# Performance work log

Hardware: AMD Instinct MI355X
Metric: run time of the kernel (lower is better)

The kernel has to match this reference:

```python
import jax, jax.numpy as jnp
import numpy as np

ALPHA = 0.2  # LeakyReLU negative slope


def setup_inputs() -> dict:
    key = jax.random.key(0)
    ks = jax.random.split(key, 8)
    B, S, T, V, F = 8, 25, 64, 256, 256
    N = S * T
    h = jax.random.normal(ks[0], (B, S, T, V), dtype=jnp.float32)
    adj = jax.random.randint(ks[1], (N, N), 0, 2, dtype=jnp.int32)
    # xavier-ish scaling for stability
    W = jax.random.normal(ks[2], (F, V), dtype=jnp.float32) * (1.414 / np.sqrt(V))
    bW = jax.random.normal(ks[3], (F,), dtype=jnp.float32) * 0.01
    ai = jax.random.normal(ks[4], (1, F), dtype=jnp.float32) * (1.414 / np.sqrt(F))
    bi = jax.random.normal(ks[5], (1,), dtype=jnp.float32) * 0.01
    aj = jax.random.normal(ks[6], (1, F), dtype=jnp.float32) * (1.414 / np.sqrt(F))
    bj = jax.random.normal(ks[7], (1,), dtype=jnp.float32) * 0.01
    return {"h": h, "adj": adj, "W": W, "bW": bW, "ai": ai, "bi": bi, "aj": aj, "bj": bj}


def reference(h, adj, W, bW, ai, bi, aj, bj):
    B, S, T, V = h.shape
    N = S * T
    x = h.reshape(B, N, V)                    # [B, N, V]
    Wh = jnp.einsum('bnv,fv->bnf', x, W) + bW  # [B, N, F]
    Wh1 = jnp.einsum('bnf,of->bno', Wh, ai) + bi  # [B, N, 1]
    Wh2 = jnp.einsum('bnf,of->bno', Wh, aj) + bj  # [B, N, 1]
    e = Wh1 + jnp.swapaxes(Wh2, 1, 2)          # [B, N, N] additive scores
    e = jnp.where(e > 0, e, ALPHA * e)         # LeakyReLU
    att = jnp.where(adj[None, :, :] > 0, e, jnp.float32(-1e9))
    att = jax.nn.softmax(att, axis=2)          # masked softmax over neighbors
    h_hat = jnp.einsum('bij,bjf->bif', att, Wh)  # [B, N, F]
    return jax.nn.elu(h_hat)                   # concat=True path
```

## Files before the change

### kernel.cpp

```cpp
#include <hip/hip_runtime.h>
#include <hip/hip_bf16.h>

typedef __attribute__((ext_vector_type(8))) short bf16x8;
typedef __attribute__((ext_vector_type(4))) float f32x4;

#define LRELU_ALPHA 0.2f

static __device__ __forceinline__ unsigned short f2bf(float x) {
    unsigned u = __float_as_uint(x);
    u += 0x7fffu + ((u >> 16) & 1u);
    return (unsigned short)(u >> 16);
}
static __device__ __forceinline__ unsigned f2ord(float x) {
    unsigned b = __float_as_uint(x);
    return (b & 0x80000000u) ? ~b : (b | 0x80000000u);
}
static __device__ __forceinline__ float ord2f(unsigned m) {
    unsigned b = (m & 0x80000000u) ? (m ^ 0x80000000u) : ~m;
    return __uint_as_float(b);
}

__global__ __launch_bounds__(256) void k_convert(
    const float* __restrict__ x, const float* __restrict__ W,
    unsigned short* __restrict__ xb, unsigned short* __restrict__ Wb)
{
    const int bid = blockIdx.x;
    const float* src;
    unsigned short* dst;
    size_t base;
    if (bid < 1600) { src = x; dst = xb; base = (size_t)bid * 2048; }
    else            { src = W; dst = Wb; base = (size_t)(bid - 1600) * 2048; }
    const size_t idx = base + (size_t)threadIdx.x * 8;
    float4 v0 = *(const float4*)&src[idx];
    float4 v1 = *(const float4*)&src[idx + 4];
    ushort4 o0 = { f2bf(v0.x), f2bf(v0.y), f2bf(v0.z), f2bf(v0.w) };
    ushort4 o1 = { f2bf(v1.x), f2bf(v1.y), f2bf(v1.z), f2bf(v1.w) };
    *(ushort4*)&dst[idx]     = o0;
    *(ushort4*)&dst[idx + 4] = o1;
}

__global__ __launch_bounds__(256) void k_gemm_fused(
    const unsigned short* __restrict__ xb, const unsigned short* __restrict__ Wb,
    const float* __restrict__ bW, const float* __restrict__ ai,
    const float* __restrict__ bi, const float* __restrict__ aj,
    const float* __restrict__ bj,
    unsigned short* __restrict__ WhT, float* __restrict__ Wh1,
    float* __restrict__ Wh2, unsigned* __restrict__ M2g)
{
    __shared__ float part1[2][32], part2[2][32];
    const int t = threadIdx.x;
    const int w = t >> 6, l = t & 63;
    const int wr = w >> 1, wc = w & 1;
    const int R0 = blockIdx.x * 32;
    const int arow = R0 + wr*16 + (l & 15);
    const int kg8 = (l >> 4) * 8;

    f32x4 acc[8];
#pragma unroll
    for (int nf = 0; nf < 8; ++nf) acc[nf] = (f32x4){0.f,0.f,0.f,0.f};

#pragma unroll 2
    for (int k0 = 0; k0 < 256; k0 += 32) {
        bf16x8 af = *(const bf16x8*)&xb[(size_t)arow*256 + k0 + kg8];
#pragma unroll
        for (int nf = 0; nf < 8; ++nf) {
            bf16x8 bfv = *(const bf16x8*)&Wb[(size_t)(wc*128 + nf*16 + (l&15))*256 + k0 + kg8];
            acc[nf] = __builtin_amdgcn_mfma_f32_16x16x32_bf16(af, bfv, acc[nf], 0, 0, 0);
        }
    }

    const int b   = R0 / 1600;
    const int n0b = R0 - b*1600;
    const int rowg = wr*16 + (l>>4)*4;
    float p1[4] = {0,0,0,0}, p2[4] = {0,0,0,0};
#pragma unroll
    for (int nf = 0; nf < 8; ++nf) {
        const int f = wc*128 + nf*16 + (l & 15);
        const float bwv = bW[f], aiv = ai[f], ajv = aj[f];
        float vv[4];
#pragma unroll
        for (int e = 0; e < 4; ++e) {
            float v = acc[nf][e] + bwv;
            vv[e] = v;
            p1[e] = __builtin_fmaf(v, aiv, p1[e]);
            p2[e] = __builtin_fmaf(v, ajv, p2[e]);
        }
        ushort4 o4 = { f2bf(vv[0]), f2bf(vv[1]), f2bf(vv[2]), f2bf(vv[3]) };
        *(ushort4*)&WhT[((size_t)(b*256 + f))*1600 + n0b + rowg] = o4;
    }
#pragma unroll
    for (int m = 1; m < 16; m <<= 1)
#pragma unroll
        for (int e = 0; e < 4; ++e) {
            p1[e] += __shfl_xor(p1[e], m, 64);
            p2[e] += __shfl_xor(p2[e], m, 64);
        }
    if ((l & 15) == 0)
#pragma unroll
        for (int e = 0; e < 4; ++e) {
            part1[wc][rowg + e] = p1[e];
            part2[wc][rowg + e] = p2[e];
        }
    __syncthreads();
    if (t < 32) {
        float v1 = part1[0][t] + part1[1][t] + bi[0];
        float v2 = part2[0][t] + part2[1][t] + bj[0];
        Wh1[R0 + t] = v1;
        Wh2[R0 + t] = v2;
        unsigned o = f2ord(v2);
#pragma unroll
        for (int m = 1; m < 32; m <<= 1) {
            unsigned o2 = __shfl_xor(o, m, 64);
            o = (o2 > o) ? o2 : o;
        }
        if (t == 0) atomicMax(&M2g[b], o);
    }
}

__global__ __launch_bounds__(512) void k_attn(
    const unsigned short* __restrict__ WhT,
    const float* __restrict__ Wh1, const unsigned* __restrict__ M2g,
    const float* __restrict__ Wh2, const int* __restrict__ adj,
    float* __restrict__ out)
{
    __shared__ alignas(16) unsigned short pls[2][32*64];
    __shared__ float l_s[32];

    const int t = threadIdx.x;
    const int w = t >> 6, l = t & 63;
    const int b = blockIdx.x & 7;
    const int i0 = (blockIdx.x >> 3) * 32;

    const float m2v = ord2f(M2g[b]);
    float wh1r[4], mr[4];
#pragma unroll
    for (int r = 0; r < 4; ++r) {
        int gi = i0 + w*4 + r;
        wh1r[r] = Wh1[b*1600 + gi];
        float s = wh1r[r] + m2v;
        mr[r] = s > 0.f ? s : LRELU_ALPHA * s;
    }
    float lsum[4] = {0.f,0.f,0.f,0.f};
    f32x4 acc[2][2];
#pragma unroll
    for (int mi = 0; mi < 2; ++mi)
#pragma unroll
        for (int nf = 0; nf < 2; ++nf) acc[mi][nf] = (f32x4){0.f,0.f,0.f,0.f};

    const unsigned short* whtb = WhT + (size_t)b*256*1600;
    const unsigned short* bp0 = whtb + (size_t)(w*32 +  0 + (l&15))*1600 + (l>>4)*8;
    const unsigned short* bp1 = whtb + (size_t)(w*32 + 16 + (l&15))*1600 + (l>>4)*8;

    int ac[4]; float wcur; bf16x8 bc[2][2];
#pragma unroll
    for (int r = 0; r < 4; ++r) ac[r] = adj[(size_t)(i0 + w*4 + r)*1600 + l];
    wcur = Wh2[b*1600 + l];
    bc[0][0] = *(const bf16x8*)(bp0);      bc[0][1] = *(const bf16x8*)(bp0 + 32);
    bc[1][0] = *(const bf16x8*)(bp1);      bc[1][1] = *(const bf16x8*)(bp1 + 32);

    for (int jt = 0; jt < 25; ++jt) {
        const int cb = jt & 1;
        int an[4]; float wn; bf16x8 bn[2][2];
        if (jt < 24) {
            const int j1 = (jt + 1) * 64;
            bn[0][0] = *(const bf16x8*)(bp0 + j1);      bn[0][1] = *(const bf16x8*)(bp0 + j1 + 32);
            bn[1][0] = *(const bf16x8*)(bp1 + j1);      bn[1][1] = *(const bf16x8*)(bp1 + j1 + 32);
#pragma unroll
            for (int r = 0; r < 4; ++r)
                an[r] = adj[(size_t)(i0 + w*4 + r)*1600 + j1 + l];
            wn = Wh2[b*1600 + j1 + l];
        }
        __builtin_amdgcn_sched_barrier(0);
#pragma unroll
        for (int r = 0; r < 4; ++r) {
            const int row = w*4 + r;
            float s = wh1r[r] + wcur;
            s = s > 0.f ? s : LRELU_ALPHA * s;
            float p = (ac[r] > 0) ? __expf(s - mr[r]) : 0.f;
            lsum[r] += p;
            int off = (row*128 + l*2) ^ ((row & 7) << 4);
            *(unsigned short*)((char*)pls[cb] + off) = f2bf(p);
        }
        asm volatile("s_waitcnt lgkmcnt(0)" ::: "memory");
        __builtin_amdgcn_sched_barrier(0);
        __builtin_amdgcn_s_barrier();
#pragma unroll
        for (int kb = 0; kb < 2; ++kb) {
            bf16x8 af[2];
#pragma unroll
            for (int mi = 0; mi < 2; ++mi) {
                int ar = mi*16 + (l & 15);
                int aoff = (ar*128 + kb*64 + (l>>4)*16) ^ ((ar & 7) << 4);
                af[mi] = *(const bf16x8*)((const char*)pls[cb] + aoff);
            }
#pragma unroll
            for (int mi = 0; mi < 2; ++mi)
#pragma unroll
                for (int nf = 0; nf < 2; ++nf)
                    acc[mi][nf] = __builtin_amdgcn_mfma_f32_16x16x32_bf16(
                        af[mi], bc[nf][kb], acc[mi][nf], 0, 0, 0);
        }
        if (jt < 24) {
#pragma unroll
            for (int r = 0; r < 4; ++r) ac[r] = an[r];
            wcur = wn;
#pragma unroll
            for (int nf = 0; nf < 2; ++nf)
#pragma unroll
                for (int kb = 0; kb < 2; ++kb) bc[nf][kb] = bn[nf][kb];
        }
    }
#pragma unroll
    for (int s2 = 1; s2 < 64; s2 <<= 1)
#pragma unroll
        for (int r = 0; r < 4; ++r)
            lsum[r] += __shfl_xor(lsum[r], s2, 64);
    if (l == 0)
#pragma unroll
        for (int r = 0; r < 4; ++r) l_s[w*4 + r] = lsum[r];
    __syncthreads();
#pragma unroll
    for (int mi = 0; mi < 2; ++mi)
#pragma unroll
        for (int e = 0; e < 4; ++e) {
            const int row = mi*16 + (l>>4)*4 + e;
            const float rl = 1.f / l_s[row];
#pragma unroll
            for (int nf = 0; nf < 2; ++nf) {
                float v = acc[mi][nf][e] * rl;
                v = v > 0.f ? v : expm1f(v);
                out[(size_t)(b*1600 + i0 + row)*256 + w*32 + nf*16 + (l & 15)] = v;
            }
        }
}

extern "C" void kernel_launch(void* const* d_in, const int* in_sizes, int n_in,
                              void* d_out, int out_size, void* d_ws, size_t ws_size,
                              hipStream_t stream)
{
    const float* h  = (const float*)d_in[0];
    const int* adj  = (const int*)d_in[1];
    const float* W  = (const float*)d_in[2];
    const float* bW = (const float*)d_in[3];
    const float* ai = (const float*)d_in[4];
    const float* bi = (const float*)d_in[5];
    const float* aj = (const float*)d_in[6];
    const float* bj = (const float*)d_in[7];
    float* out = (float*)d_out;

    char* ws = (char*)d_ws;
    unsigned short* xb  = (unsigned short*)ws;
    unsigned short* Wb  = (unsigned short*)(ws + 6553600);
    unsigned short* WhT = (unsigned short*)(ws + 6684672);
    float* Wh1 = (float*)(ws + 13238272);
    float* Wh2 = (float*)(ws + 13289472);
    unsigned* M2g = (unsigned*)(ws + 13340672);

    hipMemsetAsync(M2g, 0, 32, stream);
    k_convert<<<1632, 256, 0, stream>>>(h, W, xb, Wb);
    k_gemm_fused<<<400, 256, 0, stream>>>(xb, Wb, bW, ai, bi, aj, bj,
                                          WhT, Wh1, Wh2, M2g);
    k_attn<<<400, 512, 0, stream>>>(WhT, Wh1, M2g, Wh2, adj, out);
}
```

Measured before the change: 162.2 us.

## Split attention over key halves with combine kernel; halve GEMM row tile

The attention kernel now splits the 25 key tiles into two halves handled by separate blocks, doubling the grid to 800 blocks. Each block writes unnormalised partial outputs and row sums to workspace, and a new final kernel adds them, normalises and applies ELU. The projection GEMM uses 16-row tiles across 800 blocks, and the attention loop is restructured into a two-stage unrolled load/compute pipeline. This targets low occupancy on a GPU with many CUs, at the cost of roughly 26 MB of extra partial-result traffic and one more launch.

```diff
diff --git a/kernel.cpp b/kernel.cpp
--- a/kernel.cpp
+++ b/kernel.cpp
@@ -47,35 +47,34 @@
     unsigned short* __restrict__ WhT, float* __restrict__ Wh1,
     float* __restrict__ Wh2, unsigned* __restrict__ M2g)
 {
-    __shared__ float part1[2][32], part2[2][32];
+    __shared__ float part1[4][16], part2[4][16];
     const int t = threadIdx.x;
     const int w = t >> 6, l = t & 63;
-    const int wr = w >> 1, wc = w & 1;
-    const int R0 = blockIdx.x * 32;
-    const int arow = R0 + wr*16 + (l & 15);
+    const int R0 = blockIdx.x * 16;
+    const int arow = R0 + (l & 15);
     const int kg8 = (l >> 4) * 8;
 
-    f32x4 acc[8];
-#pragma unroll
-    for (int nf = 0; nf < 8; ++nf) acc[nf] = (f32x4){0.f,0.f,0.f,0.f};
-
-#pragma unroll 2
+    f32x4 acc[4];
+#pragma unroll
+    for (int nf = 0; nf < 4; ++nf) acc[nf] = (f32x4){0.f,0.f,0.f,0.f};
+
+#pragma unroll
     for (int k0 = 0; k0 < 256; k0 += 32) {
         bf16x8 af = *(const bf16x8*)&xb[(size_t)arow*256 + k0 + kg8];
 #pragma unroll
-        for (int nf = 0; nf < 8; ++nf) {
-            bf16x8 bfv = *(const bf16x8*)&Wb[(size_t)(wc*128 + nf*16 + (l&15))*256 + k0 + kg8];
+        for (int nf = 0; nf < 4; ++nf) {
+            bf16x8 bfv = *(const bf16x8*)&Wb[(size_t)(w*64 + nf*16 + (l&15))*256 + k0 + kg8];
             acc[nf] = __builtin_amdgcn_mfma_f32_16x16x32_bf16(af, bfv, acc[nf], 0, 0, 0);
         }
     }
 
     const int b   = R0 / 1600;
     const int n0b = R0 - b*1600;
-    const int rowg = wr*16 + (l>>4)*4;
+    const int rowg = (l >> 4) * 4;
     float p1[4] = {0,0,0,0}, p2[4] = {0,0,0,0};
 #pragma unroll
-    for (int nf = 0; nf < 8; ++nf) {
-        const int f = wc*128 + nf*16 + (l & 15);
+    for (int nf = 0; nf < 4; ++nf) {
+        const int f = w*64 + nf*16 + (l & 15);
         const float bwv = bW[f], aiv = ai[f], ajv = aj[f];
         float vv[4];
 #pragma unroll
@@ -98,22 +97,74 @@
     if ((l & 15) == 0)
 #pragma unroll
         for (int e = 0; e < 4; ++e) {
-            part1[wc][rowg + e] = p1[e];
-            part2[wc][rowg + e] = p2[e];
+            part1[w][rowg + e] = p1[e];
+            part2[w][rowg + e] = p2[e];
         }
     __syncthreads();
-    if (t < 32) {
-        float v1 = part1[0][t] + part1[1][t] + bi[0];
-        float v2 = part2[0][t] + part2[1][t] + bj[0];
+    if (t < 16) {
+        float v1 = part1[0][t]+part1[1][t]+part1[2][t]+part1[3][t] + bi[0];
+        float v2 = part2[0][t]+part2[1][t]+part2[2][t]+part2[3][t] + bj[0];
         Wh1[R0 + t] = v1;
         Wh2[R0 + t] = v2;
         unsigned o = f2ord(v2);
 #pragma unroll
-        for (int m = 1; m < 32; m <<= 1) {
+        for (int m = 1; m < 16; m <<= 1) {
             unsigned o2 = __shfl_xor(o, m, 64);
             o = (o2 > o) ? o2 : o;
         }
         if (t == 0) atomicMax(&M2g[b], o);
+    }
+}
+
+struct Tile { bf16x8 B[2][2]; int a[4]; float wv; };
+
+static __device__ __forceinline__ void load_tile(
+    Tile& S, int jt, const unsigned short* bp0, const unsigned short* bp1,
+    const int* ap, const float* wh2p, int w)
+{
+    const int j0 = jt * 64;
+    S.B[0][0] = *(const bf16x8*)(bp0 + j0);
+    S.B[0][1] = *(const bf16x8*)(bp0 + j0 + 32);
+    S.B[1][0] = *(const bf16x8*)(bp1 + j0);
+    S.B[1][1] = *(const bf16x8*)(bp1 + j0 + 32);
+#pragma unroll
+    for (int r = 0; r < 4; ++r)
+        S.a[r] = ap[(size_t)(w*4 + r)*1600 + j0];
+    S.wv = wh2p[j0];
+}
+
+static __device__ __forceinline__ void comp_tile(
+    const Tile& S, unsigned short* pb, const float* wh1r, const float* mr,
+    float* lsum, f32x4 (&acc)[2][2], int w, int l)
+{
+#pragma unroll
+    for (int r = 0; r < 4; ++r) {
+        const int row = w*4 + r;
+        float s = wh1r[r] + S.wv;
+        s = s > 0.f ? s : LRELU_ALPHA * s;
+        float p = (S.a[r] > 0) ? __expf(s - mr[r]) : 0.f;
+        lsum[r] += p;
+        int off = (row*128 + l*2) ^ ((row & 7) << 4);
+        *(unsigned short*)((char*)pb + off) = f2bf(p);
+    }
+    asm volatile("s_waitcnt lgkmcnt(0)" ::: "memory");
+    __builtin_amdgcn_sched_barrier(0);
+    __builtin_amdgcn_s_barrier();
+#pragma unroll
+    for (int kb = 0; kb < 2; ++kb) {
+        bf16x8 af[2];
+#pragma unroll
+        for (int mi = 0; mi < 2; ++mi) {
+            int ar = mi*16 + (l & 15);
+            int aoff = (ar*128 + kb*64 + (l>>4)*16) ^ ((ar & 7) << 4);
+            af[mi] = *(const bf16x8*)((const char*)pb + aoff);
+        }
+#pragma unroll
+        for (int mi = 0; mi < 2; ++mi)
+#pragma unroll
+            for (int nf = 0; nf < 2; ++nf)
+                acc[mi][nf] = __builtin_amdgcn_mfma_f32_16x16x32_bf16(
+                    af[mi], S.B[nf][kb], acc[mi][nf], 0, 0, 0);
     }
 }
 
@@ -121,15 +172,20 @@
     const unsigned short* __restrict__ WhT,
     const float* __restrict__ Wh1, const unsigned* __restrict__ M2g,
     const float* __restrict__ Wh2, const int* __restrict__ adj,
-    float* __restrict__ out)
+    float* __restrict__ Oacc, float* __restrict__ Lacc)
 {
     __shared__ alignas(16) unsigned short pls[2][32*64];
-    __shared__ float l_s[32];
 
     const int t = threadIdx.x;
     const int w = t >> 6, l = t & 63;
-    const int b = blockIdx.x & 7;
-    const int i0 = (blockIdx.x >> 3) * 32;
+    const int b  = blockIdx.x & 7;
+    const int r3 = blockIdx.x >> 3;
+    const int js = (r3 >= 50) ? 1 : 0;
+    const int gx = r3 - js*50;
+    const int i0 = gx * 32;
+    const int ggid = b*50 + gx;
+    const int t0   = js ? 13 : 0;
+    const int tend = js ? 25 : 13;
 
     const float m2v = ord2f(M2g[b]);
     float wh1r[4], mr[4];
@@ -150,66 +206,23 @@
     const unsigned short* whtb = WhT + (size_t)b*256*1600;
     const unsigned short* bp0 = whtb + (size_t)(w*32 +  0 + (l&15))*1600 + (l>>4)*8;
     const unsigned short* bp1 = whtb + (size_t)(w*32 + 16 + (l&15))*1600 + (l>>4)*8;
-
-    int ac[4]; float wcur; bf16x8 bc[2][2];
-#pragma unroll
-    for (int r = 0; r < 4; ++r) ac[r] = adj[(size_t)(i0 + w*4 + r)*1600 + l];
-    wcur = Wh2[b*1600 + l];
-    bc[0][0] = *(const bf16x8*)(bp0);      bc[0][1] = *(const bf16x8*)(bp0 + 32);
-    bc[1][0] = *(const bf16x8*)(bp1);      bc[1][1] = *(const bf16x8*)(bp1 + 32);
-
-    for (int jt = 0; jt < 25; ++jt) {
-        const int cb = jt & 1;
-        int an[4]; float wn; bf16x8 bn[2][2];
-        if (jt < 24) {
-            const int j1 = (jt + 1) * 64;
-            bn[0][0] = *(const bf16x8*)(bp0 + j1);      bn[0][1] = *(const bf16x8*)(bp0 + j1 + 32);
-            bn[1][0] = *(const bf16x8*)(bp1 + j1);      bn[1][1] = *(const bf16x8*)(bp1 + j1 + 32);
-#pragma unroll
-            for (int r = 0; r < 4; ++r)
-                an[r] = adj[(size_t)(i0 + w*4 + r)*1600 + j1 + l];
-            wn = Wh2[b*1600 + j1 + l];
-        }
+    const int*   ap   = adj + (size_t)i0*1600 + l;
+    const float* wh2p = Wh2 + b*1600 + l;
+
+    Tile S0, S1;
+    load_tile(S0, t0, bp0, bp1, ap, wh2p, w);
+    int jt = t0;
+    for (; jt + 1 < tend; jt += 2) {
+        load_tile(S1, jt + 1, bp0, bp1, ap, wh2p, w);
         __builtin_amdgcn_sched_barrier(0);
-#pragma unroll
-        for (int r = 0; r < 4; ++r) {
-            const int row = w*4 + r;
-            float s = wh1r[r] + wcur;
-            s = s > 0.f ? s : LRELU_ALPHA * s;
-            float p = (ac[r] > 0) ? __expf(s - mr[r]) : 0.f;
-            lsum[r] += p;
-            int off = (row*128 + l*2) ^ ((row & 7) << 4);
-            *(unsigned short*)((char*)pls[cb] + off) = f2bf(p);
-        }
-        asm volatile("s_waitcnt lgkmcnt(0)" ::: "memory");
+        comp_tile(S0, pls[0], wh1r, mr, lsum, acc, w, l);
+        if (jt + 2 < tend) load_tile(S0, jt + 2, bp0, bp1, ap, wh2p, w);
         __builtin_amdgcn_sched_barrier(0);
-        __builtin_amdgcn_s_barrier();
-#pragma unroll
-        for (int kb = 0; kb < 2; ++kb) {
-            bf16x8 af[2];
-#pragma unroll
-            for (int mi = 0; mi < 2; ++mi) {
-                int ar = mi*16 + (l & 15);
-                int aoff = (ar*128 + kb*64 + (l>>4)*16) ^ ((ar & 7) << 4);
-                af[mi] = *(const bf16x8*)((const char*)pls[cb] + aoff);
-            }
-#pragma unroll
-            for (int mi = 0; mi < 2; ++mi)
-#pragma unroll
-                for (int nf = 0; nf < 2; ++nf)
-                    acc[mi][nf] = __builtin_amdgcn_mfma_f32_16x16x32_bf16(
-                        af[mi], bc[nf][kb], acc[mi][nf], 0, 0, 0);
-        }
-        if (jt < 24) {
-#pragma unroll
-            for (int r = 0; r < 4; ++r) ac[r] = an[r];
-            wcur = wn;
-#pragma unroll
-            for (int nf = 0; nf < 2; ++nf)
-#pragma unroll
-                for (int kb = 0; kb < 2; ++kb) bc[nf][kb] = bn[nf][kb];
-        }
-    }
+        comp_tile(S1, pls[1], wh1r, mr, lsum, acc, w, l);
+    }
+    if (jt < tend)
+        comp_tile(S0, pls[0], wh1r, mr, lsum, acc, w, l);
+
 #pragma unroll
     for (int s2 = 1; s2 < 64; s2 <<= 1)
 #pragma unroll
@@ -217,21 +230,47 @@
             lsum[r] += __shfl_xor(lsum[r], s2, 64);
     if (l == 0)
 #pragma unroll
-        for (int r = 0; r < 4; ++r) l_s[w*4 + r] = lsum[r];
-    __syncthreads();
+        for (int r = 0; r < 4; ++r)
+            Lacc[js*12800 + ggid*32 + w*4 + r] = lsum[r];
+
+    float* ob = Oacc + ((size_t)js*400 + ggid) * 8192;
 #pragma unroll
     for (int mi = 0; mi < 2; ++mi)
 #pragma unroll
         for (int e = 0; e < 4; ++e) {
             const int row = mi*16 + (l>>4)*4 + e;
-            const float rl = 1.f / l_s[row];
-#pragma unroll
-            for (int nf = 0; nf < 2; ++nf) {
-                float v = acc[mi][nf][e] * rl;
-                v = v > 0.f ? v : expm1f(v);
-                out[(size_t)(b*1600 + i0 + row)*256 + w*32 + nf*16 + (l & 15)] = v;
-            }
-        }
+#pragma unroll
+            for (int nf = 0; nf < 2; ++nf)
+                ob[row*256 + w*32 + nf*16 + (l & 15)] = acc[mi][nf][e];
+        }
+}
+
+__global__ __launch_bounds__(256) void k_final(
+    const float* __restrict__ Oacc, const float* __restrict__ Lacc,
+    float* __restrict__ out)
+{
+    const int g = blockIdx.x;
+    const int b = g / 50, i0 = (g % 50) * 32;
+    const int t = threadIdx.x;
+    const int row = t >> 3, f0 = (t & 7) * 32;
+    const float L = Lacc[g*32 + row] + Lacc[12800 + g*32 + row];
+    const float rl = 1.f / L;
+    const float* o0 = Oacc + (size_t)g*8192 + row*256 + f0;
+    const float* o1 = o0 + 3276800;
+    float* op = out + ((size_t)(b*1600 + i0 + row))*256 + f0;
+#pragma unroll
+    for (int q = 0; q < 8; ++q) {
+        float4 a = *(const float4*)&o0[q*4];
+        float4 c = *(const float4*)&o1[q*4];
+        float v0 = (a.x + c.x) * rl, v1 = (a.y + c.y) * rl;
+        float v2 = (a.z + c.z) * rl, v3 = (a.w + c.w) * rl;
+        float4 r;
+        r.x = v0 > 0.f ? v0 : expm1f(v0);
+        r.y = v1 > 0.f ? v1 : expm1f(v1);
+        r.z = v2 > 0.f ? v2 : expm1f(v2);
+        r.w = v3 > 0.f ? v3 : expm1f(v3);
+        *(float4*)&op[q*4] = r;
+    }
 }
 
 extern "C" void kernel_launch(void* const* d_in, const int* in_sizes, int n_in,
@@ -255,10 +294,13 @@
     float* Wh1 = (float*)(ws + 13238272);
     float* Wh2 = (float*)(ws + 13289472);
     unsigned* M2g = (unsigned*)(ws + 13340672);
+    float* Oacc = (float*)(ws + 13340800);
+    float* Lacc = (float*)(ws + 39555200);
 
     hipMemsetAsync(M2g, 0, 32, stream);
     k_convert<<<1632, 256, 0, stream>>>(h, W, xb, Wb);
-    k_gemm_fused<<<400, 256, 0, stream>>>(xb, Wb, bW, ai, bi, aj, bj,
+    k_gemm_fused<<<800, 256, 0, stream>>>(xb, Wb, bW, ai, bi, aj, bj,
                                           WhT, Wh1, Wh2, M2g);
-    k_attn<<<400, 512, 0, stream>>>(WhT, Wh1, M2g, Wh2, adj, out);
-}
+    k_attn<<<800, 512, 0, stream>>>(WhT, Wh1, M2g, Wh2, adj, Oacc, Lacc);
+    k_final<<<400, 256, 0, stream>>>(Oacc, Lacc, out);
+}
```

Measured after the change: 182.9 us. +12.8%, slower.
